# Performance work log

Hardware: AMD Instinct MI355X
Metric: run time of the kernel (lower is better)

Reference implementation:

```python
import jax, jax.numpy as jnp
import numpy as np

B, S, D, H, L, DFF, NA = 128, 52, 1024, 16, 8, 4096, 1000
DK = D // H
KTOP = int((1.0 - 0.9) * S)  # per-row top-k kept before threshold = 5
EPS = 1e-5
SCALE = 1.0 / np.sqrt(DK).astype(np.float32)


def setup_inputs() -> dict:
    key = jax.random.key(0)
    ks = jax.random.split(key, 30)
    # token grid: channels 0,1 in [0,50) so only designated positions match special tokens
    x = jax.random.randint(ks[0], (B, S, 3), 0, 50).astype(jnp.int32)
    act = jax.random.randint(ks[1], (B, S), 0, NA).astype(jnp.int32)
    x = x.at[..., 2].set(act)
    x = x.at[:, 0].set(jnp.array([100, 0, 1], jnp.int32))    # SOS
    x = x.at[:, 26].set(jnp.array([100, 0, 2], jnp.int32))   # SEP
    x = x.at[:, 48:].set(jnp.array([100, 0, 0], jnp.int32))  # PAD tail

    def n(k, shape, scale=0.02):
        return (jax.random.normal(k, shape) * scale).astype(jnp.float32)

    return dict(
        x=x,
        action_emb=n(ks[2], (NA, D), 1.0),
        sep_token=n(ks[3], (D,), 1.0),
        bn_gamma=jnp.ones((S,), jnp.float32),
        bn_beta=jnp.zeros((S,), jnp.float32),
        Wq=n(ks[4], (L, D, D)), bq=jnp.zeros((L, D), jnp.float32),
        Wk=n(ks[5], (L, D, D)), bk=jnp.zeros((L, D), jnp.float32),
        Wv=n(ks[6], (L, D, D)), bv=jnp.zeros((L, D), jnp.float32),
        Wo=n(ks[7], (L, D, D)), bo=jnp.zeros((L, D), jnp.float32),
        W1=n(ks[8], (L, DFF, D)), b1=jnp.zeros((L, DFF), jnp.float32),
        W2=n(ks[9], (L, D, DFF)), b2=jnp.zeros((L, D), jnp.float32),
        ln1_g=jnp.ones((L, D), jnp.float32), ln1_b=jnp.zeros((L, D), jnp.float32),
        ln2_g=jnp.ones((L, D), jnp.float32), ln2_b=jnp.zeros((L, D), jnp.float32),
        Wout=n(ks[10], (3, D)), bout=jnp.zeros((3,), jnp.float32),
    )


def _ln(x, g, b):
    m = x.mean(-1, keepdims=True)
    v = x.var(-1, keepdims=True)
    return (x - m) * jax.lax.rsqrt(v + EPS) * g + b


def reference(x, action_emb, sep_token, bn_gamma, bn_beta,
              Wq, bq, Wk, bk, Wv, bv, Wo, bo,
              W1, b1, W2, b2, ln1_g, ln1_b, ln2_g, ln2_b, Wout, bout):
    PAD = jnp.array([100, 0, 0], x.dtype)
    SEP = jnp.array([100, 0, 2], x.dtype)
    pad = jnp.all(x == PAD, -1)            # [B,S]
    sep = jnp.all(x == SEP, -1)            # [B,S]
    valid = ~pad                            # attend only to non-pad keys

    # token-scatter embedding: sep positions -> sep_token, everything else -> action embedding
    h = jnp.where(sep[..., None], sep_token, action_emb[x[..., 2]])  # [B,S,D]

    # BatchNorm1d(52) over seq-as-channel dim (training-mode batch stats)
    mu = h.mean((0, 2), keepdims=True)
    var = h.var((0, 2), keepdims=True)
    h = (h - mu) * jax.lax.rsqrt(var + EPS) * bn_gamma[None, :, None] + bn_beta[None, :, None]

    for l in range(L):
        q = (h @ Wq[l].T + bq[l]).reshape(B, S, H, DK).transpose(0, 2, 1, 3)
        k = (h @ Wk[l].T + bk[l]).reshape(B, S, H, DK).transpose(0, 2, 1, 3)
        v = (h @ Wv[l].T + bv[l]).reshape(B, S, H, DK).transpose(0, 2, 1, 3)
        scores = jnp.einsum('bhqd,bhkd->bhqk', q, k) * SCALE       # [B,H,S,S]
        scores = jnp.where(valid[:, None, None, :], scores, -1e9)
        thr = jax.lax.top_k(scores, KTOP)[0][..., -1:]              # per-row k-th largest
        sparse = scores * (scores >= thr).astype(scores.dtype)      # zero out sub-threshold
        attn = jax.nn.softmax(sparse, axis=-1)
        o = jnp.einsum('bhqk,bhkd->bhqd', attn, v).transpose(0, 2, 1, 3).reshape(B, S, D)
        o = o @ Wo[l].T + bo[l]
        h = _ln(h + o, ln1_g[l], ln1_b[l])
        f = jax.nn.relu(h @ W1[l].T + b1[l]) @ W2[l].T + b2[l]
        h = _ln(h + f, ln2_g[l], ln2_b[l])

    y = h @ Wout.T + bout                                           # [B,S,3]
    return y[:, -1]
```

## Files before the change

### kernel.cpp

```cpp
#include <hip/hip_runtime.h>
#include <cstddef>
#include <cstdint>

#define B_    128
#define S_    52
#define D_    1024
#define H_    16
#define L_    8
#define DFF_  4096
#define DK_   64
#define T_    (B_*S_)
#define EPS_  1e-5f
#define SCALE_ 0.125f

typedef unsigned short ushortx4 __attribute__((ext_vector_type(4)));
typedef short  bf16x8 __attribute__((ext_vector_type(8)));
typedef float  f32x4  __attribute__((ext_vector_type(4)));

__device__ __forceinline__ unsigned short f2b(float f) {
  unsigned int u = __builtin_bit_cast(unsigned int, f);
  u = u + 0x7fffu + ((u >> 16) & 1u);
  return (unsigned short)(u >> 16);
}
__device__ __forceinline__ float b2f(unsigned short b) {
  unsigned int u = ((unsigned int)b) << 16;
  return __builtin_bit_cast(float, u);
}
__device__ __forceinline__ void gload16(const void* g, void* l) {
  __builtin_amdgcn_global_load_lds((const __attribute__((address_space(1))) unsigned int*)g,
      (__attribute__((address_space(3))) unsigned int*)l, 16, 0, 0);
}

__global__ __launch_bounds__(256) void k_embed(const int* __restrict__ x,
    const float* __restrict__ aemb, const float* __restrict__ sept,
    float* __restrict__ h, float* __restrict__ part, int* __restrict__ mask)
{
  int row = blockIdx.x;
  int b = row / S_;
  int s = row - b * S_;
  const int* xr = x + (size_t)row * 3;
  int x0 = xr[0], x1 = xr[1], x2 = xr[2];
  bool issep = (x0 == 100) && (x1 == 0) && (x2 == 2);
  bool ispad = (x0 == 100) && (x1 == 0) && (x2 == 0);
  int t = threadIdx.x;
  if (t == 0) mask[row] = ispad ? 0 : 1;
  const float* src = issep ? sept : (aemb + (size_t)x2 * D_);
  size_t base = (size_t)row * D_;
  float s1 = 0.f, s2 = 0.f;
#pragma unroll
  for (int i = 0; i < 4; ++i) {
    int d = t + i * 256;
    float v = src[d];
    h[base + d] = v;
    s1 += v;
    s2 += v * v;
  }
#pragma unroll
  for (int off = 32; off; off >>= 1) {
    s1 += __shfl_down(s1, off);
    s2 += __shfl_down(s2, off);
  }
  __shared__ float red[8];
  int lane = t & 63, wid = t >> 6;
  if (lane == 0) { red[wid] = s1; red[4 + wid] = s2; }
  __syncthreads();
  if (t == 0) {
    part[(size_t)s * B_ + b]        = red[0] + red[1] + red[2] + red[3];
    part[(size_t)(S_ + s) * B_ + b] = red[4] + red[5] + red[6] + red[7];
  }
}

__global__ __launch_bounds__(128) void k_bn_reduce(const float* __restrict__ part,
                                                   float* __restrict__ stats)
{
  int s = blockIdx.x;
  int t = threadIdx.x;
  float s1 = part[(size_t)s * B_ + t];
  float s2 = part[(size_t)(S_ + s) * B_ + t];
#pragma unroll
  for (int off = 32; off; off >>= 1) {
    s1 += __shfl_down(s1, off);
    s2 += __shfl_down(s2, off);
  }
  __shared__ float red[4];
  int lane = t & 63, wid = t >> 6;
  if (lane == 0) { red[wid] = s1; red[2 + wid] = s2; }
  __syncthreads();
  if (t == 0) {
    stats[s]      = red[0] + red[1];
    stats[S_ + s] = red[2] + red[3];
  }
}

__global__ __launch_bounds__(256) void k_bn_apply(float* __restrict__ h,
    const float* __restrict__ stats, const float* __restrict__ g,
    const float* __restrict__ bb, unsigned short* __restrict__ hb)
{
  int row = blockIdx.x;
  int s = row % S_;
  const float cnt = (float)(B_ * D_);
  float mu  = stats[s] / cnt;
  float var = stats[S_ + s] / cnt - mu * mu;
  float sc  = rsqrtf(var + EPS_) * g[s];
  float off = bb[s] - mu * sc;
  size_t base = (size_t)row * D_;
  int t = threadIdx.x;
#pragma unroll
  for (int i = 0; i < 4; ++i) {
    int d = t + i * 256;
    float v = h[base + d] * sc + off;
    h[base + d] = v;
    hb[base + d] = f2b(v);
  }
}

__global__ __launch_bounds__(256) void k_wconv(
    const float* __restrict__ wq, const float* __restrict__ wk,
    const float* __restrict__ wv, const float* __restrict__ wo,
    const float* __restrict__ w1, const float* __restrict__ w2,
    unsigned short* __restrict__ out)
{
  const size_t DD = (size_t)D_ * D_;
  const size_t DF = (size_t)DFF_ * D_;
  const size_t total = 4 * DD + 2 * DF;
  size_t stride = (size_t)gridDim.x * 256 * 4;
  for (size_t i = ((size_t)blockIdx.x * 256 + threadIdx.x) * 4; i < total; i += stride) {
    const float* src; size_t off;
    if      (i < DD)          { src = wq; off = i; }
    else if (i < 2 * DD)      { src = wk; off = i - DD; }
    else if (i < 3 * DD)      { src = wv; off = i - 2 * DD; }
    else if (i < 4 * DD)      { src = wo; off = i - 3 * DD; }
    else if (i < 4 * DD + DF) { src = w1; off = i - 4 * DD; }
    else                      { src = w2; off = i - 4 * DD - DF; }
    float4 v = *reinterpret_cast<const float4*>(src + off);
    ushortx4 o = { f2b(v.x), f2b(v.y), f2b(v.z), f2b(v.w) };
    *reinterpret_cast<ushortx4*>(out + i) = o;
  }
}

__global__ __launch_bounds__(256) void k_bcat(const float* __restrict__ bq,
    const float* __restrict__ bk, const float* __restrict__ bv,
    float* __restrict__ out)
{
  int i = blockIdx.x * 256 + threadIdx.x;
  int l = i / 3072, j = i - l * 3072;
  float v = (j < D_) ? bq[l * D_ + j] : (j < 2 * D_) ? bk[l * D_ + j - D_]
                                                     : bv[l * D_ + j - 2 * D_];
  out[i] = v;
}

template<int RELU, int OUTBF16>
__global__ __launch_bounds__(512, 1) void k_gemm8(
    const unsigned short* __restrict__ A, const unsigned short* __restrict__ Wt,
    const float* __restrict__ bias, void* __restrict__ C,
    int Mtiles, int Ntiles, int K, int ldc)
{
  __shared__ unsigned short lds[2 * 24576];
  const int tid = threadIdx.x;
  const int w = tid >> 6, l = tid & 63;

  const int nwg = Mtiles * Ntiles;
  int id = blockIdx.x;
  int swz = (id & 7) * (nwg >> 3) + (id >> 3);
  int bym = swz % Mtiles, bxn = swz / Mtiles;
  const int bm = bym * 256, bn = bxn * 128;

  const int colsw = 16 * ((l & 3) ^ ((l >> 2) & 3));
  const char* gA = (const char*)A + ((size_t)(bm + w * 16 + (l >> 2)) * K) * 2 + colsw;
  const char* gB = (const char*)Wt + ((size_t)(bn + w * 16 + (l >> 2)) * K) * 2 + colsw;
  const size_t rA = (size_t)128 * K * 2;
  unsigned short* lA = lds + w * 512;
  unsigned short* lB = lds + 16384 + w * 512;

#define STAGEG(g_) do {                                         \
    int tt_ = (g_) >> 1, kh_ = (g_) & 1, bb_ = tt_ & 1;         \
    size_t ko_ = (size_t)tt_ * 128 + (size_t)kh_ * 64;          \
    unsigned short* la_ = lA + bb_ * 24576 + kh_ * 8192;        \
    unsigned short* lb_ = lB + bb_ * 24576 + kh_ * 4096;        \
    gload16(gA + ko_,      la_);                                \
    gload16(gA + ko_ + rA, la_ + 4096);                         \
    gload16(gB + ko_,      lb_);                                \
  } while (0)

  const int fr = l & 15, kg = l >> 4;
  const int wr = w >> 1, wc = w & 1;
  const int xr = 16 * (kg ^ (fr & 3));
  const int aBase = (wr * 64 + fr) * 64 + xr;
  const int bBase = 32768 + (wc * 64 + fr) * 64 + xr;

  f32x4 acc[4][4] = {};
  const int NPH = K >> 5;

  STAGEG(0); STAGEG(1); STAGEG(2);
  asm volatile("s_waitcnt vmcnt(6)" ::: "memory");
  __builtin_amdgcn_sched_barrier(0);
  __builtin_amdgcn_s_barrier();
  __builtin_amdgcn_sched_barrier(0);

  for (int g = 0; g < NPH; ++g) {
    if (g + 3 < NPH) STAGEG(g + 3);
    const char* bp = (const char*)lds + ((g >> 1) & 1) * 49152;
    const int kh = g & 1;
    bf16x8 af[4], bfv[4];
#pragma unroll
    for (int mf = 0; mf < 4; ++mf)
      af[mf] = *(const bf16x8*)(bp + kh * 16384 + aBase + mf * 1024);
#pragma unroll
    for (int nf = 0; nf < 4; ++nf)
      bfv[nf] = *(const bf16x8*)(bp + kh * 8192 + bBase + nf * 1024);
    __builtin_amdgcn_s_setprio(1);
    asm volatile("s_waitcnt lgkmcnt(0)" ::: "memory");
    __builtin_amdgcn_sched_barrier(0);
#pragma unroll
    for (int mf = 0; mf < 4; ++mf)
#pragma unroll
      for (int nf = 0; nf < 4; ++nf)
        acc[mf][nf] = __builtin_amdgcn_mfma_f32_16x16x32_bf16(af[mf], bfv[nf], acc[mf][nf], 0, 0, 0);
    __builtin_amdgcn_s_setprio(0);
    __builtin_amdgcn_sched_barrier(0);
    if (g + 1 < NPH) {
      if (g < NPH - 3)       { asm volatile("s_waitcnt vmcnt(6)" ::: "memory"); }
      else if (g == NPH - 3) { asm volatile("s_waitcnt vmcnt(3)" ::: "memory"); }
      else                   { asm volatile("s_waitcnt vmcnt(0)" ::: "memory"); }
      __builtin_amdgcn_sched_barrier(0);
      __builtin_amdgcn_s_barrier();
      __builtin_amdgcn_sched_barrier(0);
    }
  }
#undef STAGEG

#pragma unroll
  for (int nf = 0; nf < 4; ++nf) {
    int col = bn + wc * 64 + nf * 16 + fr;
    float bv = bias[col];
#pragma unroll
    for (int mf = 0; mf < 4; ++mf) {
      int row0 = bm + wr * 64 + mf * 16 + kg * 4;
#pragma unroll
      for (int j = 0; j < 4; ++j) {
        float v = acc[mf][nf][j] + bv;
        if (RELU) v = fmaxf(v, 0.f);
        if (OUTBF16)
          ((unsigned short*)C)[(size_t)(row0 + j) * ldc + col] = f2b(v);
        else
          ((float*)C)[(size_t)(row0 + j) * ldc + col] = v;
      }
    }
  }
}

__global__ __launch_bounds__(64) void k_attn(const unsigned short* __restrict__ qkv,
    const int* __restrict__ mask, unsigned short* __restrict__ ao)
{
  __shared__ float sc[64][68];
  __shared__ unsigned short ph[64][68];
  __shared__ unsigned short plo[64][68];
  __shared__ unsigned short vT[64][68];
  __shared__ float dnm[64];

  int blk = blockIdx.x;
  int b = blk >> 4, hh = blk & 15;
  int l = threadIdx.x;
  int cl = l & 15, kg = l >> 4;
  const unsigned short* base = qkv + (size_t)(b * S_) * 3072 + hh * 64;

  {
    const unsigned short* vp = base + 2048 + l;
#pragma unroll 4
    for (int k = 0; k < S_; ++k)
      vT[l][k] = vp[(size_t)k * 3072];
#pragma unroll
    for (int k = S_; k < 64; ++k) vT[l][k] = 0;
  }

  bf16x8 qa[4][2], kb[4][2];
#pragma unroll
  for (int mi = 0; mi < 4; ++mi) {
    int row = mi * 16 + cl;
    bool ok = (row < S_);
    const unsigned short* qp = base + (size_t)row * 3072 + kg * 8;
#pragma unroll
    for (int ks = 0; ks < 2; ++ks) {
      bf16x8 z = {};
      qa[mi][ks] = ok ? *reinterpret_cast<const bf16x8*>(qp + ks * 32) : z;
      kb[mi][ks] = ok ? *reinterpret_cast<const bf16x8*>(qp + 1024 + ks * 32) : z;
    }
  }

  f32x4 acc[4][4] = {};
#pragma unroll
  for (int ks = 0; ks < 2; ++ks)
#pragma unroll
    for (int mi = 0; mi < 4; ++mi)
#pragma unroll
      for (int ci = 0; ci < 4; ++ci)
        acc[mi][ci] = __builtin_amdgcn_mfma_f32_16x16x32_bf16(qa[mi][ks], kb[ci][ks], acc[mi][ci], 0, 0, 0);

  int vld[4];
#pragma unroll
  for (int ci = 0; ci < 4; ++ci) {
    int col = ci * 16 + cl;
    vld[ci] = (col < S_) ? mask[b * S_ + col] : 0;
  }
#pragma unroll
  for (int mi = 0; mi < 4; ++mi)
#pragma unroll
    for (int ci = 0; ci < 4; ++ci)
#pragma unroll
      for (int j = 0; j < 4; ++j)
        sc[mi * 16 + kg * 4 + j][ci * 16 + cl] = vld[ci] ? acc[mi][ci][j] * SCALE_ : -1e9f;

  __syncthreads();

  if (l < S_) {
    float v0 = -3e38f, v1 = -3e38f, v2 = -3e38f, v3 = -3e38f, v4 = -3e38f;
    const float4* rp = reinterpret_cast<const float4*>(&sc[l][0]);
#pragma unroll
    for (int c4 = 0; c4 < 13; ++c4) {
      float4 x = rp[c4];
      float xs[4] = { x.x, x.y, x.z, x.w };
#pragma unroll
      for (int u = 0; u < 4; ++u) {
        float xv = xs[u];
        if      (xv > v0) { v4 = v3; v3 = v2; v2 = v1; v1 = v0; v0 = xv; }
        else if (xv > v1) { v4 = v3; v3 = v2; v2 = v1; v1 = xv; }
        else if (xv > v2) { v4 = v3; v3 = v2; v2 = xv; }
        else if (xv > v3) { v4 = v3; v3 = xv; }
        else if (xv > v4) { v4 = xv; }
      }
    }
    float thr = v4;
    float m = fmaxf(v0, 0.f);
    float denom = 0.f;
    for (int c = 0; c < S_; ++c) {
      float xv = sc[l][c];
      float sp = (xv >= thr) ? xv : 0.f;
      float e = __expf(sp - m);
      denom += e;
      unsigned short hi = f2b(e);
      ph[l][c] = hi;
      plo[l][c] = f2b(e - b2f(hi));
    }
#pragma unroll
    for (int c = S_; c < 64; ++c) { ph[l][c] = 0; plo[l][c] = 0; }
    dnm[l] = 1.f / denom;
  }
  __syncthreads();

  f32x4 o[4][4] = {};
#pragma unroll
  for (int ks = 0; ks < 2; ++ks) {
    bf16x8 vf[4];
#pragma unroll
    for (int di = 0; di < 4; ++di)
      vf[di] = *reinterpret_cast<const bf16x8*>(&vT[di * 16 + cl][ks * 32 + kg * 8]);
#pragma unroll
    for (int mi = 0; mi < 4; ++mi) {
      bf16x8 ahi = *reinterpret_cast<const bf16x8*>(&ph[mi * 16 + cl][ks * 32 + kg * 8]);
      bf16x8 alo = *reinterpret_cast<const bf16x8*>(&plo[mi * 16 + cl][ks * 32 + kg * 8]);
#pragma unroll
      for (int di = 0; di < 4; ++di) {
        o[mi][di] = __builtin_amdgcn_mfma_f32_16x16x32_bf16(ahi, vf[di], o[mi][di], 0, 0, 0);
        o[mi][di] = __builtin_amdgcn_mfma_f32_16x16x32_bf16(alo, vf[di], o[mi][di], 0, 0, 0);
      }
    }
  }

#pragma unroll
  for (int mi = 0; mi < 4; ++mi) {
    int row = mi * 16 + kg * 4;
    if (row < S_) {
#pragma unroll
      for (int j = 0; j < 4; ++j) {
        int r = row + j;
        float inv = dnm[r];
        unsigned short* aop = ao + (size_t)(b * S_ + r) * D_ + hh * DK_;
#pragma unroll
        for (int di = 0; di < 4; ++di)
          aop[di * 16 + cl] = f2b(o[mi][di][j] * inv);
      }
    }
  }
}

__global__ __launch_bounds__(256) void k_add_ln(float* __restrict__ h,
    const float* __restrict__ r, const float* __restrict__ g,
    const float* __restrict__ bb, unsigned short* __restrict__ hb)
{
  int row = blockIdx.x;
  size_t base = (size_t)row * D_;
  int t = threadIdx.x;
  float xs[4];
  float s1 = 0.f, s2 = 0.f;
#pragma unroll
  for (int i = 0; i < 4; ++i) {
    int d = t + i * 256;
    float xv = h[base + d] + r[base + d];
    xs[i] = xv;
    s1 += xv;
    s2 += xv * xv;
  }
#pragma unroll
  for (int off = 32; off; off >>= 1) {
    s1 += __shfl_down(s1, off);
    s2 += __shfl_down(s2, off);
  }
  __shared__ float red[8];
  int lane = t & 63, wid = t >> 6;
  if (lane == 0) { red[wid] = s1; red[4 + wid] = s2; }
  __syncthreads();
  if (t == 0) {
    red[0] = red[0] + red[1] + red[2] + red[3];
    red[4] = red[4] + red[5] + red[6] + red[7];
  }
  __syncthreads();
  float mean = red[0] / (float)D_;
  float var  = red[4] / (float)D_ - mean * mean;
  float inv  = rsqrtf(var + EPS_);
#pragma unroll
  for (int i = 0; i < 4; ++i) {
    int d = t + i * 256;
    float v = (xs[i] - mean) * inv * g[d] + bb[d];
    h[base + d] = v;
    hb[base + d] = f2b(v);
  }
}

__global__ __launch_bounds__(256) void k_final(const float* __restrict__ h,
    const float* __restrict__ Wout, const float* __restrict__ bout,
    float* __restrict__ y)
{
  int b = blockIdx.x;
  const float* hr = h + (size_t)(b * S_ + (S_ - 1)) * D_;
  int t = threadIdx.x;
  float p0 = 0.f, p1 = 0.f, p2 = 0.f;
  for (int d = t; d < D_; d += 256) {
    float xv = hr[d];
    p0 += xv * Wout[d];
    p1 += xv * Wout[D_ + d];
    p2 += xv * Wout[2 * D_ + d];
  }
#pragma unroll
  for (int off = 32; off; off >>= 1) {
    p0 += __shfl_down(p0, off);
    p1 += __shfl_down(p1, off);
    p2 += __shfl_down(p2, off);
  }
  __shared__ float red[12];
  int lane = t & 63, wid = t >> 6;
  if (lane == 0) { red[wid] = p0; red[4 + wid] = p1; red[8 + wid] = p2; }
  __syncthreads();
  if (t == 0) {
    y[b * 3 + 0] = red[0] + red[1] + red[2]  + red[3]  + bout[0];
    y[b * 3 + 1] = red[4] + red[5] + red[6]  + red[7]  + bout[1];
    y[b * 3 + 2] = red[8] + red[9] + red[10] + red[11] + bout[2];
  }
}

extern "C" void kernel_launch(void* const* d_in, const int* in_sizes, int n_in,
                              void* d_out, int out_size, void* d_ws, size_t ws_size,
                              hipStream_t stream)
{
  const int*   x    = (const int*)d_in[0];
  const float* aemb = (const float*)d_in[1];
  const float* sept = (const float*)d_in[2];
  const float* bng  = (const float*)d_in[3];
  const float* bnb  = (const float*)d_in[4];
  const float* Wq = (const float*)d_in[5];  const float* bq = (const float*)d_in[6];
  const float* Wk = (const float*)d_in[7];  const float* bk = (const float*)d_in[8];
  const float* Wv = (const float*)d_in[9];  const float* bv = (const float*)d_in[10];
  const float* Wo = (const float*)d_in[11]; const float* bo = (const float*)d_in[12];
  const float* W1 = (const float*)d_in[13]; const float* b1 = (const float*)d_in[14];
  const float* W2 = (const float*)d_in[15]; const float* b2 = (const float*)d_in[16];
  const float* ln1g = (const float*)d_in[17]; const float* ln1b = (const float*)d_in[18];
  const float* ln2g = (const float*)d_in[19]; const float* ln2b = (const float*)d_in[20];
  const float* Wout = (const float*)d_in[21]; const float* bout = (const float*)d_in[22];
  float* out = (float*)d_out;

  float* ws = (float*)d_ws;
  const size_t TD = (size_t)T_ * D_;
  const size_t DD = (size_t)D_ * D_;
  const size_t DF = (size_t)DFF_ * D_;
  float* h   = ws;
  float* tmp = ws + TD;
  unsigned short* hb   = (unsigned short*)(ws + 2 * TD);
  unsigned short* qkvb = (unsigned short*)(ws + 2 * TD + TD / 2);
  unsigned short* aob  = (unsigned short*)(ws + 4 * TD);
  unsigned short* ffb  = (unsigned short*)(ws + 4 * TD + TD / 2);
  unsigned short* wbuf = (unsigned short*)(ws + 6 * TD + TD / 2);
  float* bqkv = ws + 6 * TD + TD / 2 + (4 * DD + 2 * DF) / 2;
  float* stats = bqkv + L_ * 3072;
  float* part  = stats + 2 * S_;
  int*   mask  = (int*)(part + 2 * S_ * B_);

  k_embed<<<T_, 256, 0, stream>>>(x, aemb, sept, h, part, mask);
  k_bn_reduce<<<S_, 128, 0, stream>>>(part, stats);
  k_bn_apply<<<T_, 256, 0, stream>>>(h, stats, bng, bnb, hb);
  k_bcat<<<(L_ * 3072) / 256, 256, 0, stream>>>(bq, bk, bv, bqkv);

  for (int l = 0; l < L_; ++l) {
    k_wconv<<<3072, 256, 0, stream>>>(Wq + l * DD, Wk + l * DD, Wv + l * DD,
                                      Wo + l * DD, W1 + l * DF, W2 + l * DF, wbuf);
    k_gemm8<0, 1><<<26 * 24, 512, 0, stream>>>(hb, wbuf, bqkv + l * 3072,
        qkvb, 26, 24, 1024, 3072);
    k_attn<<<B_ * H_, 64, 0, stream>>>(qkvb, mask, aob);
    k_gemm8<0, 0><<<26 * 8, 512, 0, stream>>>(aob, wbuf + 3 * DD, bo + l * D_,
        tmp, 26, 8, 1024, 1024);
    k_add_ln<<<T_, 256, 0, stream>>>(h, tmp, ln1g + l * D_, ln1b + l * D_, hb);
    k_gemm8<1, 1><<<26 * 32, 512, 0, stream>>>(hb, wbuf + 4 * DD, b1 + l * DFF_,
        ffb, 26, 32, 1024, 4096);
    k_gemm8<0, 0><<<26 * 8, 512, 0, stream>>>(ffb, wbuf + 4 * DD + DF, b2 + l * D_,
        tmp, 26, 8, 4096, 1024);
    k_add_ln<<<T_, 256, 0, stream>>>(h, tmp, ln2g + l * D_, ln2b + l * D_, hb);
  }
  k_final<<<B_, 256, 0, stream>>>(h, Wout, bout, out);
}
```

Baseline: 2.933 ms.

## Restructure GEMM to triple-buffered 32-wide K stages with smaller LDS footprint

```diff
diff --git a/kernel.cpp b/kernel.cpp
--- a/kernel.cpp
+++ b/kernel.cpp
@@ -150,12 +150,12 @@
 }
 
 template<int RELU, int OUTBF16>
-__global__ __launch_bounds__(512, 1) void k_gemm8(
+__global__ __launch_bounds__(512, 4) void k_gemm8(
     const unsigned short* __restrict__ A, const unsigned short* __restrict__ Wt,
     const float* __restrict__ bias, void* __restrict__ C,
     int Mtiles, int Ntiles, int K, int ldc)
 {
-  __shared__ unsigned short lds[2 * 24576];
+  __shared__ unsigned short lds[3 * 12288];
   const int tid = threadIdx.x;
   const int w = tid >> 6, l = tid & 63;
 
@@ -165,52 +165,55 @@
   int bym = swz % Mtiles, bxn = swz / Mtiles;
   const int bm = bym * 256, bn = bxn * 128;
 
-  const int colsw = 16 * ((l & 3) ^ ((l >> 2) & 3));
-  const char* gA = (const char*)A + ((size_t)(bm + w * 16 + (l >> 2)) * K) * 2 + colsw;
+  const int colsw = 16 * ((l & 3) ^ ((l >> 3) & 3));
+  const char* gA = (const char*)A + ((size_t)(bm + w * 32 + (l >> 2)) * K) * 2 + colsw;
   const char* gB = (const char*)Wt + ((size_t)(bn + w * 16 + (l >> 2)) * K) * 2 + colsw;
-  const size_t rA = (size_t)128 * K * 2;
-  unsigned short* lA = lds + w * 512;
-  unsigned short* lB = lds + 16384 + w * 512;
-
-#define STAGEG(g_) do {                                         \
-    int tt_ = (g_) >> 1, kh_ = (g_) & 1, bb_ = tt_ & 1;         \
-    size_t ko_ = (size_t)tt_ * 128 + (size_t)kh_ * 64;          \
-    unsigned short* la_ = lA + bb_ * 24576 + kh_ * 8192;        \
-    unsigned short* lb_ = lB + bb_ * 24576 + kh_ * 4096;        \
-    gload16(gA + ko_,      la_);                                \
-    gload16(gA + ko_ + rA, la_ + 4096);                         \
-    gload16(gB + ko_,      lb_);                                \
+  const size_t r16 = (size_t)16 * K * 2;
+  unsigned short* lA = lds + w * 1024;
+  unsigned short* lB = lds + 8192 + w * 512;
+
+#define STAGE(tt, bb) do {                          \
+    size_t ko_ = (size_t)(tt) * 64;                 \
+    unsigned short* la_ = lA + (bb) * 12288;        \
+    unsigned short* lb_ = lB + (bb) * 12288;        \
+    gload16(gA + ko_,       la_);                   \
+    gload16(gA + ko_ + r16, la_ + 512);             \
+    gload16(gB + ko_,       lb_);                   \
   } while (0)
 
   const int fr = l & 15, kg = l >> 4;
   const int wr = w >> 1, wc = w & 1;
-  const int xr = 16 * (kg ^ (fr & 3));
-  const int aBase = (wr * 64 + fr) * 64 + xr;
-  const int bBase = 32768 + (wc * 64 + fr) * 64 + xr;
+  const int xk = 16 * (kg ^ ((fr >> 1) & 3));
+  const int aOff = (wr * 64 + fr) * 64 + xk;
+  const int bOff = 16384 + (wc * 64 + fr) * 64 + xk;
 
   f32x4 acc[4][4] = {};
-  const int NPH = K >> 5;
-
-  STAGEG(0); STAGEG(1); STAGEG(2);
-  asm volatile("s_waitcnt vmcnt(6)" ::: "memory");
-  __builtin_amdgcn_sched_barrier(0);
-  __builtin_amdgcn_s_barrier();
-  __builtin_amdgcn_sched_barrier(0);
-
-  for (int g = 0; g < NPH; ++g) {
-    if (g + 3 < NPH) STAGEG(g + 3);
-    const char* bp = (const char*)lds + ((g >> 1) & 1) * 49152;
-    const int kh = g & 1;
+  const int NT = K >> 5;
+
+  STAGE(0, 0);
+  STAGE(1, 1);
+  int cur = 0;
+  for (int t = 0; t < NT; ++t) {
+    if (t + 1 < NT) { asm volatile("s_waitcnt vmcnt(3)" ::: "memory"); }
+    else            { asm volatile("s_waitcnt vmcnt(0)" ::: "memory"); }
+    __builtin_amdgcn_sched_barrier(0);
+    __builtin_amdgcn_s_barrier();
+    __builtin_amdgcn_sched_barrier(0);
+    if (t + 2 < NT) {
+      int nb = cur + 2; if (nb >= 3) nb -= 3;
+      STAGE(t + 2, nb);
+    }
+    const char* bp = (const char*)lds + cur * 24576;
     bf16x8 af[4], bfv[4];
 #pragma unroll
     for (int mf = 0; mf < 4; ++mf)
-      af[mf] = *(const bf16x8*)(bp + kh * 16384 + aBase + mf * 1024);
+      af[mf] = *(const bf16x8*)(bp + aOff + mf * 1024);
 #pragma unroll
     for (int nf = 0; nf < 4; ++nf)
-      bfv[nf] = *(const bf16x8*)(bp + kh * 8192 + bBase + nf * 1024);
-    __builtin_amdgcn_s_setprio(1);
+      bfv[nf] = *(const bf16x8*)(bp + bOff + nf * 1024);
     asm volatile("s_waitcnt lgkmcnt(0)" ::: "memory");
     __builtin_amdgcn_sched_barrier(0);
+    __builtin_amdgcn_s_setprio(1);
 #pragma unroll
     for (int mf = 0; mf < 4; ++mf)
 #pragma unroll
@@ -218,16 +221,9 @@
         acc[mf][nf] = __builtin_amdgcn_mfma_f32_16x16x32_bf16(af[mf], bfv[nf], acc[mf][nf], 0, 0, 0);
     __builtin_amdgcn_s_setprio(0);
     __builtin_amdgcn_sched_barrier(0);
-    if (g + 1 < NPH) {
-      if (g < NPH - 3)       { asm volatile("s_waitcnt vmcnt(6)" ::: "memory"); }
-      else if (g == NPH - 3) { asm volatile("s_waitcnt vmcnt(3)" ::: "memory"); }
-      else                   { asm volatile("s_waitcnt vmcnt(0)" ::: "memory"); }
-      __builtin_amdgcn_sched_barrier(0);
-      __builtin_amdgcn_s_barrier();
-      __builtin_amdgcn_sched_barrier(0);
-    }
-  }
-#undef STAGEG
+    cur = (cur == 2) ? 0 : cur + 1;
+  }
+#undef STAGE
 
 #pragma unroll
   for (int nf = 0; nf < 4; ++nf) {
```

New measurement: 2.587 ms. -11.8%, faster.
